# Optimization experiments

Measured on AMD Instinct MI355X. Metric: run time of the kernel, lower is better.

## Reference

```python
import jax, jax.numpy as jnp
import numpy as np

K_RADIUS = 1            # 2k+1 = 3 neighborhood -> 9 offsets
AFF_THRESH = 0.5        # affinity = 1/(1+dist); edge iff affinity > 0.5 (dist < 1)
N_PROP_STEPS = 40       # label propagation iterations
M_PARENTS = 256         # max parent segments per image (num_nodes of next level)


def _offsets(k):
    return [(dy, dx) for dy in range(-k, k + 1) for dx in range(-k, k + 1)]


def _shift2d(x, dy, dx, fill):
    """Shift spatial dims (axes 1,2) of x by (dy,dx), padding with `fill`."""
    kr = K_RADIUS
    pad = [(0, 0), (kr, kr), (kr, kr)] + [(0, 0)] * (x.ndim - 3)
    xp = jnp.pad(x, pad, constant_values=fill)
    H, W = x.shape[1], x.shape[2]
    return xp[:, kr + dy:kr + dy + H, kr + dx:kr + dx + W]


def setup_inputs() -> dict:
    key = jax.random.key(0)
    features = jax.random.normal(key, (32, 128, 128, 64), dtype=jnp.float32)
    return {"features": features}


def reference(features):
    BT, H, W, C = features.shape
    N = H * W
    offs = _offsets(K_RADIUS)

    # ---- compute_affinities: inverse Euclidean distance in (2k+1)^2 window ----
    aff_list = []
    for dy, dx in offs:
        nb = _shift2d(features, dy, dx, fill=1e6)  # out-of-bounds -> huge dist -> aff ~ 0
        dist = jnp.sqrt(jnp.sum((features - nb) ** 2, axis=-1) + 1e-12)
        aff_list.append(1.0 / (1.0 + dist))
    affinities = jnp.stack(aff_list, axis=-1)      # [BT,H,W,K]

    # ---- threshold_affinities ----
    edges = affinities > AFF_THRESH                # [BT,H,W,K] bool

    # ---- compute_parents: label propagation (min-label flooding over edges) ----
    labels0 = jnp.broadcast_to(
        jnp.arange(N, dtype=jnp.int32).reshape(1, H, W), (BT, H, W))
    SENT = jnp.int32(N)  # sentinel larger than any label

    def body(_, lab):
        cands = [lab]
        for j, (dy, dx) in enumerate(offs):
            nb = _shift2d(lab, dy, dx, fill=N)
            cands.append(jnp.where(edges[..., j], nb, SENT))
        return jnp.min(jnp.stack(cands, axis=0), axis=0)

    labels = jax.lax.fori_loop(0, N_PROP_STEPS, body, labels0)  # [BT,H,W]
    lab_flat = labels.reshape(BT, N)

    # ---- register_parents: relabel to contiguous ids, capped at M (preproc_segment_ids) ----
    def relabel(lab):
        present = jnp.zeros((N,), jnp.int32).at[lab].set(1)
        rank = jnp.cumsum(present) - 1
        return jnp.minimum(rank[lab], M_PARENTS - 1)

    seg = jax.vmap(relabel)(lab_flat)              # [BT,N] in [0,M)

    # ---- aggregate_nodes_and_features: per-segment mean and variance ----
    flat_ids = (seg + jnp.arange(BT, dtype=jnp.int32)[:, None] * M_PARENTS).reshape(-1)
    feat = features.reshape(BT * N, C)
    sums = jax.ops.segment_sum(feat, flat_ids, num_segments=BT * M_PARENTS)
    sqs = jax.ops.segment_sum(feat * feat, flat_ids, num_segments=BT * M_PARENTS)
    cnt = jax.ops.segment_sum(jnp.ones((BT * N, 1), feat.dtype), flat_ids,
                              num_segments=BT * M_PARENTS)
    denom = jnp.maximum(cnt, 1.0)
    mean = sums / denom
    var = jnp.maximum(sqs / denom - mean * mean, 0.0)
    parent_nodes = jnp.concatenate([mean, var], axis=-1).reshape(BT, M_PARENTS, 2 * C)
    return parent_nodes
```

## Files before the change

### kernel.cpp

```cpp
#include <hip/hip_runtime.h>
#include <stdint.h>

#define HH 128
#define WW 128
#define NPIX 16384
#define BTN 32
#define CCH 64
#define MPAR 256
#define SENT 16384
#define NSTEPS 40

#define ETX 32
#define ETY 8
__global__ __launch_bounds__(256) void edge_kernel(const float* __restrict__ feat,
                                                   unsigned char* __restrict__ mask4,
                                                   float4* __restrict__ accz,
                                                   float4* __restrict__ cntz) {
  __shared__ float lds[8][308];
  int blk = blockIdx.x;
  int tid = threadIdx.x;

  if (tid < 128) accz[blk * 128 + tid] = make_float4(0.f, 0.f, 0.f, 0.f);
  else if (tid == 128) cntz[blk] = make_float4(0.f, 0.f, 0.f, 0.f);

  int b = blk >> 6;
  int t = blk & 63;
  int ty0 = (t >> 2) * ETY;
  int tx0 = (t & 3) * ETX;
  const float* fb = feat + ((size_t)b << 20);

  for (int sp = tid; sp < 306; sp += 256) {
    int gy = ty0 + sp / 34;
    int gx = tx0 - 1 + sp % 34;
    if (gy < HH && (unsigned)gx < (unsigned)WW) {
      const float* pp = fb + (((size_t)(gy << 7) + gx) << 6);
      float4 v0 = *(const float4*)pp;
      float4 v1 = *(const float4*)(pp + 4);
      lds[0][sp] = v0.x; lds[1][sp] = v0.y; lds[2][sp] = v0.z; lds[3][sp] = v0.w;
      lds[4][sp] = v1.x; lds[5][sp] = v1.y; lds[6][sp] = v1.z; lds[7][sp] = v1.w;
    } else {
#pragma unroll
      for (int c = 0; c < 8; ++c) lds[c][sp] = 1e6f;
    }
  }
  __syncthreads();

  int tx = tid & 31, ty = tid >> 5;
  int idx = ty * 34 + tx + 1;
  int gx = tx0 + tx, gy = ty0 + ty;

  float own[8];
#pragma unroll
  for (int c = 0; c < 8; ++c) own[c] = lds[c][idx];
  float a0 = 0.f, a1 = 0.f, a2 = 0.f, a3 = 0.f;
#pragma unroll
  for (int c = 0; c < 8; ++c) {
    float o = own[c];
    float d0 = o - lds[c][idx + 1];
    float d1 = o - lds[c][idx + 33];
    float d2 = o - lds[c][idx + 34];
    float d3 = o - lds[c][idx + 35];
    a0 += d0 * d0; a1 += d1 * d1; a2 += d2 * d2; a3 += d3 * d3;
  }

  bool vS = (gy + 1) < HH;
  float acc[4] = {a0, a1, a2, a3};
  bool val[4] = {(gx + 1) < WW, vS && gx >= 1, vS, vS && (gx + 1) < WW};
  const int offp[4] = {1, 127, 128, 129};
  const float* fp = fb + (((size_t)(gy << 7) + gx) << 6);
  unsigned m = 0;
#pragma unroll
  for (int j = 0; j < 4; ++j) {
    if (val[j]) {
      float s = acc[j];
      if (s < 1.0f) {
        const float* np_ = fp + ((size_t)offp[j] << 6);
        for (int c = 8; c < 64; ++c) {
          float d = fp[c] - np_[c];
          s += d * d;
        }
      }
      if (s + 1e-12f < 1.0f) m |= (1u << j);
    }
  }
  mask4[(b << 14) + (gy << 7) + gx] = (unsigned char)m;
}

__global__ __launch_bounds__(1024) void prop_kernel(const unsigned char* __restrict__ mask4g,
                                                    unsigned char* __restrict__ segg) {
  __shared__ __align__(16) unsigned short lab[NPIX];
  __shared__ __align__(16) unsigned char e8[NPIX];
  __shared__ __align__(16) unsigned short rnk[NPIX];
  __shared__ int flags[2];
  __shared__ int wsum[16];
  __shared__ int wexc[16];
  __shared__ int wany[16];
  int b = blockIdx.x;
  int tid = threadIdx.x;
  int lane = tid & 63, wid = tid >> 6;

  uint4 mv = ((const uint4*)(mask4g + ((size_t)b << 14)))[tid];
  ((uint4*)e8)[tid] = mv;
  unsigned anyv = mv.x | mv.y | mv.z | mv.w;
  unsigned long long bal = __ballot(anyv != 0);
  if (lane == 0) wany[wid] = (bal != 0ull) ? 1 : 0;
  __syncthreads();

  int tot = 0;
#pragma unroll
  for (int i = 0; i < 16; ++i) tot |= wany[i];
  if (tot == 0) {
    uint4 w;
    if (tid < 16) {
      unsigned b0 = (unsigned)(tid * 16);
      w.x = b0 | ((b0 + 1) << 8) | ((b0 + 2) << 16) | ((b0 + 3) << 24);
      w.y = (b0 + 4) | ((b0 + 5) << 8) | ((b0 + 6) << 16) | ((b0 + 7) << 24);
      w.z = (b0 + 8) | ((b0 + 9) << 8) | ((b0 + 10) << 16) | ((b0 + 11) << 24);
      w.w = (b0 + 12) | ((b0 + 13) << 8) | ((b0 + 14) << 16) | ((b0 + 15) << 24);
    } else {
      w = make_uint4(~0u, ~0u, ~0u, ~0u);
    }
    ((uint4*)(segg + ((size_t)b << 14)))[tid] = w;
    return;
  }

  unsigned char tmp[16];
  {
    int base = tid * 16;
#pragma unroll
    for (int i = 0; i < 16; ++i) {
      int p = base + i;
      int y = p >> 7, x = p & (WW - 1);
      unsigned own = e8[p];
      unsigned nw = (y > 0 && x > 0) ? e8[p - 129] : 0;
      unsigned n_ = (y > 0) ? e8[p - 128] : 0;
      unsigned ne = (y > 0 && x < WW - 1) ? e8[p - 127] : 0;
      unsigned w_ = (x > 0) ? e8[p - 1] : 0;
      unsigned v = ((nw >> 3) & 1) | (((n_ >> 2) & 1) << 1) | (((ne >> 1) & 1) << 2) |
                   ((w_ & 1) << 3) | ((own & 1) << 4) | (((own >> 1) & 1) << 5) |
                   (((own >> 2) & 1) << 6) | (((own >> 3) & 1) << 7);
      tmp[i] = (unsigned char)v;
    }
  }
  __syncthreads();
  {
    int base = tid * 16;
#pragma unroll
    for (int i = 0; i < 16; ++i) e8[base + i] = tmp[i];
#pragma unroll
    for (int i = 0; i < 16; ++i) lab[base + i] = (unsigned short)(base + i);
  }
  if (tid == 0) { flags[0] = 0; flags[1] = 0; }
  __syncthreads();

  int x0 = (tid & 31) * 4, y0 = (tid >> 5) * 4;
  int cur[4][4], eb[4][4];
#pragma unroll
  for (int r = 0; r < 4; ++r)
#pragma unroll
    for (int c = 0; c < 4; ++c) {
      cur[r][c] = (y0 + r) * WW + x0 + c;
      eb[r][c] = e8[(y0 + r) * WW + x0 + c];
    }

  for (int it = 0; it < NSTEPS; ++it) {
    int top[6], bot[6], lft[4], rgt[4];
#pragma unroll
    for (int c = 0; c < 6; ++c) {
      top[c] = lab[(((y0 - 1) * WW) + x0 - 1 + c) & (NPIX - 1)];
      bot[c] = lab[(((y0 + 4) * WW) + x0 - 1 + c) & (NPIX - 1)];
    }
#pragma unroll
    for (int r = 0; r < 4; ++r) {
      lft[r] = lab[(((y0 + r) * WW) + x0 - 1) & (NPIX - 1)];
      rgt[r] = lab[(((y0 + r) * WW) + x0 + 4) & (NPIX - 1)];
    }
    int nl[4][4];
    bool ch = false;
#pragma unroll
    for (int r = 0; r < 4; ++r) {
#pragma unroll
      for (int c = 0; c < 4; ++c) {
        int m = cur[r][c];
        int e = eb[r][c];
        int v;
        v = (r > 0) ? ((c > 0) ? cur[r - 1][c - 1] : lft[r - 1]) : top[c];
        m = min(m, (e & 1) ? v : SENT);
        v = (r > 0) ? cur[r - 1][c] : top[c + 1];
        m = min(m, (e & 2) ? v : SENT);
        v = (r > 0) ? ((c < 3) ? cur[r - 1][c + 1] : rgt[r - 1]) : top[c + 2];
        m = min(m, (e & 4) ? v : SENT);
        v = (c > 0) ? cur[r][c - 1] : lft[r];
        m = min(m, (e & 8) ? v : SENT);
        v = (c < 3) ? cur[r][c + 1] : rgt[r];
        m = min(m, (e & 16) ? v : SENT);
        v = (r < 3) ? ((c > 0) ? cur[r + 1][c - 1] : lft[r + 1]) : bot[c];
        m = min(m, (e & 32) ? v : SENT);
        v = (r < 3) ? cur[r + 1][c] : bot[c + 1];
        m = min(m, (e & 64) ? v : SENT);
        v = (r < 3) ? ((c < 3) ? cur[r + 1][c + 1] : rgt[r + 1]) : bot[c + 2];
        m = min(m, (e & 128) ? v : SENT);
        nl[r][c] = m;
        ch |= (m != cur[r][c]);
      }
    }
    __syncthreads();
#pragma unroll
    for (int r = 0; r < 4; ++r) {
      unsigned lo = (unsigned)nl[r][0] | ((unsigned)nl[r][1] << 16);
      unsigned hi = (unsigned)nl[r][2] | ((unsigned)nl[r][3] << 16);
      *((uint2*)&lab[(y0 + r) * WW + x0]) = make_uint2(lo, hi);
    }
    if (ch) flags[it & 1] = 1;
    if (tid == 0) flags[(it + 1) & 1] = 0;
#pragma unroll
    for (int r = 0; r < 4; ++r)
#pragma unroll
      for (int c = 0; c < 4; ++c) cur[r][c] = nl[r][c];
    __syncthreads();
    if (!flags[it & 1]) break;
  }

  __syncthreads();
  ((uint4*)e8)[tid] = make_uint4(0u, 0u, 0u, 0u);
  __syncthreads();
#pragma unroll
  for (int i = 0; i < 16; ++i) {
    int p = tid + i * 1024;
    e8[lab[p]] = 1;
  }
  __syncthreads();
  int pres[16];
  int base = tid * 16;
#pragma unroll
  for (int i = 0; i < 16; ++i) pres[i] = e8[base + i];
  int s_local = 0;
#pragma unroll
  for (int i = 0; i < 16; ++i) s_local += pres[i];
  int inc = s_local;
#pragma unroll
  for (int off = 1; off < 64; off <<= 1) {
    int v = __shfl_up(inc, off, 64);
    if (lane >= off) inc += v;
  }
  if (lane == 63) wsum[wid] = inc;
  __syncthreads();
  if (wid == 0) {
    int tt = (lane < 16) ? wsum[lane] : 0;
    int winc = tt;
#pragma unroll
    for (int off = 1; off < 16; off <<= 1) {
      int v = __shfl_up(winc, off, 64);
      if (lane >= off) winc += v;
    }
    if (lane < 16) wexc[lane] = winc - tt;
  }
  __syncthreads();
  int run = wexc[wid] + (inc - s_local);
#pragma unroll
  for (int i = 0; i < 16; ++i) {
    run += pres[i];
    rnk[base + i] = (unsigned short)(run - 1);
  }
  __syncthreads();
  unsigned char* so = segg + ((size_t)b << 14);
#pragma unroll
  for (int i = 0; i < 16; ++i) {
    int p = tid + i * 1024;
    int sg = rnk[lab[p]];
    so[p] = (unsigned char)min(sg, 255);
  }
}

#define PXW 128
__global__ __launch_bounds__(256) void agg_kernel(const float* __restrict__ feat,
                                                  const unsigned char* __restrict__ segg,
                                                  float* __restrict__ acc,
                                                  float* __restrict__ cnt) {
  int lane = threadIdx.x & 63;
  int gw = blockIdx.x * 4 + (threadIdx.x >> 6);
  int b = gw >> 7;
  int chunk = gw & 127;
  int basep = (b << 14) + (chunk << 7);
  const unsigned char* sp = segg + basep;
  int s0 = sp[lane];
  int s1 = sp[64 + lane];
  const float* fp = feat + ((size_t)basep << 6) + lane;

  float sacc = 0.f, qacc = 0.f, cacc = 0.f;
  int curs = __builtin_amdgcn_readlane(s0, 0);

  float v[32];
#pragma unroll
  for (int u = 0; u < 32; ++u) v[u] = fp[(size_t)u << 6];

#pragma unroll
  for (int kk = 0; kk < PXW; kk += 32) {
    float w[32];
    if (kk + 32 < PXW) {
#pragma unroll
      for (int u = 0; u < 32; ++u) w[u] = fp[(size_t)(kk + 32 + u) << 6];
    }
#pragma unroll
    for (int u = 0; u < 32; ++u) {
      int k = kk + u;
      int sg = __builtin_amdgcn_readlane((k & 64) ? s1 : s0, k & 63);
      if (sg != curs) {
        float* a = acc + ((size_t)((b << 8) + curs) << 7);
        atomicAdd(a + lane, sacc);
        atomicAdd(a + 64 + lane, qacc);
        if (lane == 0) atomicAdd(cnt + (b << 8) + curs, cacc);
        curs = sg; sacc = 0.f; qacc = 0.f; cacc = 0.f;
      }
      sacc += v[u]; qacc += v[u] * v[u]; cacc += 1.f;
    }
#pragma unroll
    for (int u = 0; u < 32; ++u) v[u] = w[u];
  }
  {
    float* a = acc + ((size_t)((b << 8) + curs) << 7);
    atomicAdd(a + lane, sacc);
    atomicAdd(a + 64 + lane, qacc);
    if (lane == 0) atomicAdd(cnt + (b << 8) + curs, cacc);
  }
}

__global__ __launch_bounds__(256) void fin_kernel(float* __restrict__ acc,
                                                  const float* __restrict__ cnt) {
  int gid = blockIdx.x * 256 + threadIdx.x;
  int bm = gid >> 6, c = gid & 63;
  float* a = acc + ((size_t)bm << 7);
  float s = a[c], q = a[c + 64];
  float n = cnt[bm];
  float denom = fmaxf(n, 1.0f);
  float mean = s / denom;
  float var = fmaxf(q / denom - mean * mean, 0.0f);
  a[c] = mean;
  a[c + 64] = var;
}

extern "C" void kernel_launch(void* const* d_in, const int* in_sizes, int n_in,
                              void* d_out, int out_size, void* d_ws, size_t ws_size,
                              hipStream_t stream) {
  const float* feat = (const float*)d_in[0];
  unsigned char* mask4 = (unsigned char*)d_ws;
  unsigned char* segg = mask4 + (size_t)BTN * NPIX;
  float* cnt = (float*)(segg + (size_t)BTN * NPIX);
  float* acc = (float*)d_out;

  edge_kernel<<<BTN * 64, 256, 0, stream>>>(feat, mask4, (float4*)acc, (float4*)cnt);
  prop_kernel<<<BTN, 1024, 0, stream>>>(mask4, segg);
  agg_kernel<<<BTN * NPIX / PXW / 4, 256, 0, stream>>>(feat, segg, acc, cnt);
  fin_kernel<<<BTN * MPAR * CCH / 256, 256, 0, stream>>>(acc, cnt);
}
```

Baseline: 217.0 us.

## Fuse per-row feature sums into edge pass and aggregate by uniform-segment rows

Result: slower. 239.4 us (+10.4%).

```diff
diff --git a/kernel.cpp b/kernel.cpp
--- a/kernel.cpp
+++ b/kernel.cpp
@@ -10,80 +10,85 @@
 #define SENT 16384
 #define NSTEPS 40
 
-#define ETX 32
-#define ETY 8
-__global__ __launch_bounds__(256) void edge_kernel(const float* __restrict__ feat,
-                                                   unsigned char* __restrict__ mask4,
-                                                   float4* __restrict__ accz,
-                                                   float4* __restrict__ cntz) {
-  __shared__ float lds[8][308];
+__global__ __launch_bounds__(256) void fused_kernel(const float* __restrict__ feat,
+                                                    unsigned char* __restrict__ mask4,
+                                                    float* __restrict__ prow) {
+  __shared__ float lm[5][128][9];
   int blk = blockIdx.x;
   int tid = threadIdx.x;
-
-  if (tid < 128) accz[blk * 128 + tid] = make_float4(0.f, 0.f, 0.f, 0.f);
-  else if (tid == 128) cntz[blk] = make_float4(0.f, 0.f, 0.f, 0.f);
-
-  int b = blk >> 6;
-  int t = blk & 63;
-  int ty0 = (t >> 2) * ETY;
-  int tx0 = (t & 3) * ETX;
-  const float* fb = feat + ((size_t)b << 20);
-
-  for (int sp = tid; sp < 306; sp += 256) {
-    int gy = ty0 + sp / 34;
-    int gx = tx0 - 1 + sp % 34;
-    if (gy < HH && (unsigned)gx < (unsigned)WW) {
-      const float* pp = fb + (((size_t)(gy << 7) + gx) << 6);
-      float4 v0 = *(const float4*)pp;
-      float4 v1 = *(const float4*)(pp + 4);
-      lds[0][sp] = v0.x; lds[1][sp] = v0.y; lds[2][sp] = v0.z; lds[3][sp] = v0.w;
-      lds[4][sp] = v1.x; lds[5][sp] = v1.y; lds[6][sp] = v1.z; lds[7][sp] = v1.w;
-    } else {
-#pragma unroll
-      for (int c = 0; c < 8; ++c) lds[c][sp] = 1e6f;
-    }
-  }
-  __syncthreads();
-
-  int tx = tid & 31, ty = tid >> 5;
-  int idx = ty * 34 + tx + 1;
-  int gx = tx0 + tx, gy = ty0 + ty;
-
-  float own[8];
-#pragma unroll
-  for (int c = 0; c < 8; ++c) own[c] = lds[c][idx];
-  float a0 = 0.f, a1 = 0.f, a2 = 0.f, a3 = 0.f;
-#pragma unroll
-  for (int c = 0; c < 8; ++c) {
-    float o = own[c];
-    float d0 = o - lds[c][idx + 1];
-    float d1 = o - lds[c][idx + 33];
-    float d2 = o - lds[c][idx + 34];
-    float d3 = o - lds[c][idx + 35];
-    a0 += d0 * d0; a1 += d1 * d1; a2 += d2 * d2; a3 += d3 * d3;
-  }
-
-  bool vS = (gy + 1) < HH;
-  float acc[4] = {a0, a1, a2, a3};
-  bool val[4] = {(gx + 1) < WW, vS && gx >= 1, vS, vS && (gx + 1) < WW};
-  const int offp[4] = {1, 127, 128, 129};
-  const float* fp = fb + (((size_t)(gy << 7) + gx) << 6);
-  unsigned m = 0;
-#pragma unroll
-  for (int j = 0; j < 4; ++j) {
-    if (val[j]) {
-      float s = acc[j];
-      if (s < 1.0f) {
-        const float* np_ = fp + ((size_t)offp[j] << 6);
-        for (int c = 8; c < 64; ++c) {
-          float d = fp[c] - np_[c];
-          s += d * d;
+  int lane = tid & 63, w = tid >> 6;
+  int b = blk >> 5;
+  int ty = (blk & 31) << 2;
+  int y = ty + w;
+
+  const float* fr = feat + (((size_t)(b << 14) + (y << 7)) << 6);
+  float sacc = 0.f, qacc = 0.f;
+  for (int p0 = 0; p0 < 128; p0 += 8) {
+    float t[8];
+#pragma unroll
+    for (int u = 0; u < 8; ++u) t[u] = fr[((p0 + u) << 6) + lane];
+#pragma unroll
+    for (int u = 0; u < 8; ++u) { sacc += t[u]; qacc += t[u] * t[u]; }
+    if (lane < 8) {
+#pragma unroll
+      for (int u = 0; u < 8; ++u) lm[w][p0 + u][lane] = t[u];
+    }
+  }
+  {
+    int px = tid >> 1, h = tid & 1;
+    int hy = ty + 4;
+    float4 v;
+    if (hy < HH)
+      v = *(const float4*)(feat + (((size_t)(b << 14) + (hy << 7) + px) << 6) + h * 4);
+    else
+      v = make_float4(1e6f, 1e6f, 1e6f, 1e6f);
+    lm[4][px][h * 4 + 0] = v.x; lm[4][px][h * 4 + 1] = v.y;
+    lm[4][px][h * 4 + 2] = v.z; lm[4][px][h * 4 + 3] = v.w;
+  }
+  float* pr = prow + (((size_t)(b << 7) + y) << 7);
+  pr[lane] = sacc;
+  pr[64 + lane] = qacc;
+  __syncthreads();
+
+#pragma unroll
+  for (int i = 0; i < 2; ++i) {
+    int p = tid + (i << 8);
+    int row = p >> 7, x = p & 127;
+    int gy = ty + row;
+    int xm = (x > 0) ? x - 1 : 0;
+    int xp = (x < 127) ? x + 1 : 127;
+    float a0 = 0.f, a1 = 0.f, a2 = 0.f, a3 = 0.f;
+#pragma unroll
+    for (int c = 0; c < 8; ++c) {
+      float o = lm[row][x][c];
+      float d0 = o - lm[row][xp][c];
+      float d1 = o - lm[row + 1][xm][c];
+      float d2 = o - lm[row + 1][x][c];
+      float d3 = o - lm[row + 1][xp][c];
+      a0 += d0 * d0; a1 += d1 * d1; a2 += d2 * d2; a3 += d3 * d3;
+    }
+    bool vS = (gy + 1) < HH;
+    float acc[4] = {a0, a1, a2, a3};
+    bool val[4] = {x < 127, vS && x > 0, vS, vS && x < 127};
+    const int offp[4] = {1, 127, 128, 129};
+    const float* fp = feat + (((size_t)(b << 14) + (gy << 7) + x) << 6);
+    unsigned m = 0;
+#pragma unroll
+    for (int j = 0; j < 4; ++j) {
+      if (val[j]) {
+        float s = acc[j];
+        if (s < 1.0f) {
+          const float* np_ = fp + ((size_t)offp[j] << 6);
+          for (int c = 8; c < 64; ++c) {
+            float d = fp[c] - np_[c];
+            s += d * d;
+          }
         }
-      }
-      if (s + 1e-12f < 1.0f) m |= (1u << j);
-    }
-  }
-  mask4[(b << 14) + (gy << 7) + gx] = (unsigned char)m;
+        if (s + 1e-12f < 1.0f) m |= (1u << j);
+      }
+    }
+    mask4[(b << 14) + (gy << 7) + x] = (unsigned char)m;
+  }
 }
 
 __global__ __launch_bounds__(1024) void prop_kernel(const unsigned char* __restrict__ mask4g,
@@ -272,71 +277,88 @@
   }
 }
 
-#define PXW 128
-__global__ __launch_bounds__(256) void agg_kernel(const float* __restrict__ feat,
+__global__ __launch_bounds__(256) void fin_kernel(const float* __restrict__ feat,
                                                   const unsigned char* __restrict__ segg,
-                                                  float* __restrict__ acc,
-                                                  float* __restrict__ cnt) {
-  int lane = threadIdx.x & 63;
-  int gw = blockIdx.x * 4 + (threadIdx.x >> 6);
-  int b = gw >> 7;
-  int chunk = gw & 127;
-  int basep = (b << 14) + (chunk << 7);
-  const unsigned char* sp = segg + basep;
-  int s0 = sp[lane];
-  int s1 = sp[64 + lane];
-  const float* fp = feat + ((size_t)basep << 6) + lane;
-
-  float sacc = 0.f, qacc = 0.f, cacc = 0.f;
-  int curs = __builtin_amdgcn_readlane(s0, 0);
-
-  float v[32];
-#pragma unroll
-  for (int u = 0; u < 32; ++u) v[u] = fp[(size_t)u << 6];
-
-#pragma unroll
-  for (int kk = 0; kk < PXW; kk += 32) {
-    float w[32];
-    if (kk + 32 < PXW) {
-#pragma unroll
-      for (int u = 0; u < 32; ++u) w[u] = fp[(size_t)(kk + 32 + u) << 6];
-    }
-#pragma unroll
-    for (int u = 0; u < 32; ++u) {
-      int k = kk + u;
-      int sg = __builtin_amdgcn_readlane((k & 64) ? s1 : s0, k & 63);
-      if (sg != curs) {
-        float* a = acc + ((size_t)((b << 8) + curs) << 7);
-        atomicAdd(a + lane, sacc);
-        atomicAdd(a + 64 + lane, qacc);
-        if (lane == 0) atomicAdd(cnt + (b << 8) + curs, cacc);
-        curs = sg; sacc = 0.f; qacc = 0.f; cacc = 0.f;
-      }
-      sacc += v[u]; qacc += v[u] * v[u]; cacc += 1.f;
-    }
-#pragma unroll
-    for (int u = 0; u < 32; ++u) v[u] = w[u];
-  }
-  {
-    float* a = acc + ((size_t)((b << 8) + curs) << 7);
-    atomicAdd(a + lane, sacc);
-    atomicAdd(a + 64 + lane, qacc);
-    if (lane == 0) atomicAdd(cnt + (b << 8) + curs, cacc);
-  }
-}
-
-__global__ __launch_bounds__(256) void fin_kernel(float* __restrict__ acc,
-                                                  const float* __restrict__ cnt) {
-  int gid = blockIdx.x * 256 + threadIdx.x;
-  int bm = gid >> 6, c = gid & 63;
-  float* a = acc + ((size_t)bm << 7);
-  float s = a[c], q = a[c + 64];
-  float n = cnt[bm];
-  float denom = fmaxf(n, 1.0f);
-  float mean = s / denom;
-  float var = fmaxf(q / denom - mean * mean, 0.0f);
-  a[c] = mean;
-  a[c + 64] = var;
+                                                  const float* __restrict__ prow,
+                                                  float* __restrict__ out) {
+  __shared__ __align__(16) float accL[MPAR][128];
+  __shared__ __align__(16) unsigned char segL[NPIX];
+  __shared__ float cntL[MPAR];
+  __shared__ short rowseg[128];
+  int b = blockIdx.x;
+  int tid = threadIdx.x;
+
+  for (int i = tid; i < MPAR * 32; i += 256) ((float4*)accL)[i] = make_float4(0.f, 0.f, 0.f, 0.f);
+  cntL[tid] = 0.f;
+  for (int i = 0; i < 16; ++i)
+    ((unsigned int*)segL)[tid + (i << 8)] = ((const unsigned int*)(segg + ((size_t)b << 14)))[tid + (i << 8)];
+  __syncthreads();
+
+  if (tid < 128) {
+    const unsigned int* rp = (const unsigned int*)(segL + (tid << 7));
+    unsigned int u0 = rp[0];
+    unsigned int sp = (u0 & 255u) * 0x01010101u;
+    bool ok = true;
+#pragma unroll
+    for (int j = 0; j < 32; ++j) ok &= (rp[j] == sp);
+    rowseg[tid] = ok ? (short)(u0 & 255u) : (short)-1;
+  }
+  __syncthreads();
+
+  if (tid < 128) {
+    int curs = -1;
+    float racc = 0.f;
+    for (int r = 0; r < 128; ++r) {
+      float v = prow[(((size_t)(b << 7) + r) << 7) + tid];
+      int s = rowseg[r];
+      if (s != curs) {
+        if (curs >= 0) accL[curs][tid] += racc;
+        curs = s; racc = 0.f;
+      }
+      if (s >= 0) racc += v;
+    }
+    if (curs >= 0) accL[curs][tid] += racc;
+    int ch = tid & 63;
+    bool issq = tid >= 64;
+    for (int r = 0; r < 128; ++r)
+      if (rowseg[r] < 0) {
+        const float* fb = feat + (((size_t)(b << 14) + (r << 7)) << 6);
+        for (int p = 0; p < 128; ++p) {
+          int s = segL[(r << 7) + p];
+          float v = fb[(p << 6) + ch];
+          accL[s][tid] += issq ? v * v : v;
+        }
+      }
+  } else if (tid == 128) {
+    int curs = -1;
+    float rc = 0.f;
+    for (int r = 0; r < 128; ++r) {
+      int s = rowseg[r];
+      if (s != curs) {
+        if (curs >= 0) cntL[curs] += rc;
+        curs = s; rc = 0.f;
+      }
+      if (s >= 0) rc += 128.f;
+    }
+    if (curs >= 0) cntL[curs] += rc;
+    for (int r = 0; r < 128; ++r)
+      if (rowseg[r] < 0)
+        for (int p = 0; p < 128; ++p) cntL[segL[(r << 7) + p]] += 1.f;
+  }
+  __syncthreads();
+
+  for (int i = 0; i < 64; ++i) {
+    int idx = tid + (i << 8);
+    int m = idx >> 6, ch = idx & 63;
+    float n = cntL[m];
+    float s = accL[m][ch], q = accL[m][ch + 64];
+    float denom = fmaxf(n, 1.0f);
+    float mean = s / denom;
+    float var = fmaxf(q / denom - mean * mean, 0.0f);
+    float* o = out + (((size_t)(b << 8) + m) << 7);
+    o[ch] = mean;
+    o[64 + ch] = var;
+  }
 }
 
 extern "C" void kernel_launch(void* const* d_in, const int* in_sizes, int n_in,
@@ -345,11 +367,10 @@
   const float* feat = (const float*)d_in[0];
   unsigned char* mask4 = (unsigned char*)d_ws;
   unsigned char* segg = mask4 + (size_t)BTN * NPIX;
-  float* cnt = (float*)(segg + (size_t)BTN * NPIX);
-  float* acc = (float*)d_out;
-
-  edge_kernel<<<BTN * 64, 256, 0, stream>>>(feat, mask4, (float4*)acc, (float4*)cnt);
+  float* prow = (float*)(segg + (size_t)BTN * NPIX);
+  float* out = (float*)d_out;
+
+  fused_kernel<<<BTN * 32, 256, 0, stream>>>(feat, mask4, prow);
   prop_kernel<<<BTN, 1024, 0, stream>>>(mask4, segg);
-  agg_kernel<<<BTN * NPIX / PXW / 4, 256, 0, stream>>>(feat, segg, acc, cnt);
-  fin_kernel<<<BTN * MPAR * CCH / 256, 256, 0, stream>>>(acc, cnt);
+  fin_kernel<<<BTN, 256, 0, stream>>>(feat, segg, prow, out);
 }
```
